# Kernel optimization log

Hardware: AMD Instinct MI355X
Metric: run time of the kernel (lower is better)

Reference implementation:

```python
import math
import jax, jax.numpy as jnp
import numpy as np

# Faithful constants from the source: angle=180 degrees
_THETA = 180.0 * math.pi / 180.0
COS_T = np.float32(math.cos(_THETA))   # -1.0
SIN_T = np.float32(math.sin(_THETA))   # ~1.2246e-16 (kept exactly as torch code does)
EPS = 1e-05


def setup_inputs() -> dict:
    key = jax.random.key(0)
    k1, k2 = jax.random.split(key)
    x = jax.random.normal(k1, (32, 256, 56, 56), dtype=jnp.float32)
    r = jax.random.normal(k2, (32, 256, 7, 7), dtype=jnp.float32)
    return {"x": x, "r": r}


def reference(x, r):
    # LRP m-rule backward pass through AdaptiveAvgPool2d.
    # H, W divisible by out_h, out_w -> every window is kh x kw, identical to the
    # floor/ceil window bounds in the original Python double loop.
    B, C, H, W = x.shape
    oh, ow = r.shape[-2], r.shape[-1]
    if (H, W) == (oh, ow):
        return r
    kh, kw = H // oh, W // ow
    k = kh * kw
    eps = jnp.float32(EPS)

    # unfold windows: [B,C,H,W] -> [N, k], N = B*C*oh*ow
    xw = x.reshape(B, C, oh, kh, ow, kw).transpose(0, 1, 2, 4, 3, 5).reshape(-1, k)
    rs = r.reshape(-1)  # [N], one relevance scalar per window (n_filters == 1)

    # averaging filter w = ones(k)/k ; its normalized version is 1/sqrt(k) each
    w = jnp.full((k,), 1.0 / k, dtype=x.dtype)
    nw = w / (jnp.sqrt(jnp.sum(w * w)) + eps)  # [k]

    norm_x = jnp.sqrt(jnp.sum(xw * xw, axis=-1, keepdims=True)) + eps  # [N,1]
    nx = xw / norm_x                                                   # [N,k]
    wx = nx @ nw                                                       # [N]

    orth = nw[None, :] - wx[:, None] * nx                              # [N,k]
    n_orth = orth / (jnp.sqrt(jnp.sum(orth * orth, axis=-1, keepdims=True)) + eps)

    x_head = (COS_T * nx + SIN_T * n_orth) * norm_x                    # [N,k]
    x_diff = xw - x_head
    wx_diff = w[None, :] * x_diff                                      # [N,k]
    out = wx_diff / (jnp.sum(wx_diff, axis=-1, keepdims=True) + eps) * rs[:, None]

    # fold back: [N,k] -> [B,C,H,W] (windows are disjoint -> no scatter-add races)
    relevance = out.reshape(B, C, oh, ow, kh, kw).transpose(0, 1, 2, 4, 3, 5).reshape(B, C, H, W)
    return relevance
```

## Files before the change

### kernel.cpp

```cpp
#include <hip/hip_runtime.h>


typedef float f32x4 __attribute__((ext_vector_type(4)));

static constexpr int HW     = 56 * 56;
static constexpr int NWIN   = 8192 * 49;
static constexpr int NGRP   = NWIN / 8;
static constexpr int BLOCKS = 1792;
static constexpr int WAVES  = BLOCKS * 4;
static constexpr int NITER  = NGRP / WAVES;

__global__ __launch_bounds__(256) void lrp_pool_kernel(
    const float* __restrict__ x,
    const float* __restrict__ r,
    float* __restrict__ out)
{
    const int tid  = threadIdx.x;
    const int lane = tid & 63;
    const int w    = lane >> 3;
    const int t    = lane & 7;

    const int g0 = blockIdx.x * 4 + (tid >> 6);

    #pragma unroll
    for (int it = 0; it < NITER; ++it) {
        const int g   = g0 + it * WAVES;
        const int wid = g * 8 + w;
        const int bc  = wid / 49;
        const int rem = wid - bc * 49;
        const int ohi = rem / 7;
        const int owi = rem - ohi * 7;

        const int base = bc * HW + (ohi * 8 + t) * 56 + owi * 8;
        const float* p = x + base;

        const f32x4 a = *reinterpret_cast<const f32x4*>(p);
        const f32x4 b = *reinterpret_cast<const f32x4*>(p + 4);
        const float rv = r[wid];

        double s = (((double)a.x + (double)a.y) + ((double)a.z + (double)a.w))
                 + (((double)b.x + (double)b.y) + ((double)b.z + (double)b.w));
        s += __shfl_xor(s, 1, 64);
        s += __shfl_xor(s, 2, 64);
        s += __shfl_xor(s, 4, 64);

        const float coef = rv / (float)(s + 32.0 * 1e-5);

        *reinterpret_cast<f32x4*>(out + base)     = a * coef;
        *reinterpret_cast<f32x4*>(out + base + 4) = b * coef;
    }
}

extern "C" void kernel_launch(void* const* d_in, const int* in_sizes, int n_in,
                              void* d_out, int out_size, void* d_ws, size_t ws_size,
                              hipStream_t stream) {
    const float* x   = (const float*)d_in[0];
    const float* r   = (const float*)d_in[1];
    float*       out = (float*)d_out;
    lrp_pool_kernel<<<BLOCKS, 256, 0, stream>>>(x, r, out);
}
```

Before: 38.46 us.

## Assign one full 8x8 window per thread instead of one row per thread

Each thread now loads a whole 8x8 window (16 float4 loads), sums it in double locally, and writes the scaled window back, in place of eight threads sharing a window and reducing through xor shuffles. This removes the cross-lane shuffles and the grid-stride loop, and the grid is sized so each wave covers 64 windows. In exchange, adjacent lanes now touch addresses 32 bytes apart in different rows, so memory coalescing is worse, and register pressure rises from holding 64 floats per thread.

```diff
diff --git a/kernel.cpp b/kernel.cpp
--- a/kernel.cpp
+++ b/kernel.cpp
@@ -4,50 +4,51 @@
 typedef float f32x4 __attribute__((ext_vector_type(4)));
 
 static constexpr int HW     = 56 * 56;
-static constexpr int NWIN   = 8192 * 49;
-static constexpr int NGRP   = NWIN / 8;
-static constexpr int BLOCKS = 1792;
-static constexpr int WAVES  = BLOCKS * 4;
-static constexpr int NITER  = NGRP / WAVES;
+static constexpr int BLOCKS = 1568;
 
 __global__ __launch_bounds__(256) void lrp_pool_kernel(
     const float* __restrict__ x,
     const float* __restrict__ r,
     float* __restrict__ out)
 {
-    const int tid  = threadIdx.x;
-    const int lane = tid & 63;
-    const int w    = lane >> 3;
-    const int t    = lane & 7;
+    const int gw   = blockIdx.x * 4 + (threadIdx.x >> 6);
+    const int lane = threadIdx.x & 63;
+    const int wid  = gw * 64 + lane;
 
-    const int g0 = blockIdx.x * 4 + (tid >> 6);
+    const int bc  = wid / 49;
+    const int rem = wid - bc * 49;
+    const int ohi = rem / 7;
+    const int owi = rem - ohi * 7;
+
+    const int base = bc * HW + (ohi * 8) * 56 + owi * 8;
+    const float* p = x + base;
+
+    f32x4 v[16];
+    #pragma unroll
+    for (int rr = 0; rr < 8; ++rr) {
+        v[2 * rr]     = *reinterpret_cast<const f32x4*>(p + rr * 56);
+        v[2 * rr + 1] = *reinterpret_cast<const f32x4*>(p + rr * 56 + 4);
+    }
+    const float rv = r[wid];
+
+    double a0 = 0.0, a1 = 0.0, a2 = 0.0, a3 = 0.0;
+    #pragma unroll
+    for (int i = 0; i < 4; ++i) {
+        const f32x4 w0 = v[4 * i + 0], w1 = v[4 * i + 1];
+        const f32x4 w2 = v[4 * i + 2], w3 = v[4 * i + 3];
+        a0 += ((double)w0.x + (double)w0.y) + ((double)w0.z + (double)w0.w);
+        a1 += ((double)w1.x + (double)w1.y) + ((double)w1.z + (double)w1.w);
+        a2 += ((double)w2.x + (double)w2.y) + ((double)w2.z + (double)w2.w);
+        a3 += ((double)w3.x + (double)w3.y) + ((double)w3.z + (double)w3.w);
+    }
+    const double s = (a0 + a1) + (a2 + a3);
+
+    const float coef = rv / (float)(s + 32.0 * 1e-5);
 
     #pragma unroll
-    for (int it = 0; it < NITER; ++it) {
-        const int g   = g0 + it * WAVES;
-        const int wid = g * 8 + w;
-        const int bc  = wid / 49;
-        const int rem = wid - bc * 49;
-        const int ohi = rem / 7;
-        const int owi = rem - ohi * 7;
-
-        const int base = bc * HW + (ohi * 8 + t) * 56 + owi * 8;
-        const float* p = x + base;
-
-        const f32x4 a = *reinterpret_cast<const f32x4*>(p);
-        const f32x4 b = *reinterpret_cast<const f32x4*>(p + 4);
-        const float rv = r[wid];
-
-        double s = (((double)a.x + (double)a.y) + ((double)a.z + (double)a.w))
-                 + (((double)b.x + (double)b.y) + ((double)b.z + (double)b.w));
-        s += __shfl_xor(s, 1, 64);
-        s += __shfl_xor(s, 2, 64);
-        s += __shfl_xor(s, 4, 64);
-
-        const float coef = rv / (float)(s + 32.0 * 1e-5);
-
-        *reinterpret_cast<f32x4*>(out + base)     = a * coef;
-        *reinterpret_cast<f32x4*>(out + base + 4) = b * coef;
+    for (int rr = 0; rr < 8; ++rr) {
+        *reinterpret_cast<f32x4*>(out + base + rr * 56)     = v[2 * rr]     * coef;
+        *reinterpret_cast<f32x4*>(out + base + rr * 56 + 4) = v[2 * rr + 1] * coef;
     }
 }
 
```

Result: slower. 43.33 us (+12.7%).
